# Kernel tuning notes

Measured on AMD Instinct MI355X. Metric: run time of the kernel, lower is better.

Reference implementation:

```python
import jax, jax.numpy as jnp
import numpy as np

L, H, D, DH, DFF, V, P, T, R = 12, 12, 768, 64, 3072, 30522, 512, 2, 50
RAT_LAYER = 6  # original condition: 5 < idx < 7


def layer_norm(x, g, b, eps=1e-12):
    m = x.mean(-1, keepdims=True)
    v = ((x - m) ** 2).mean(-1, keepdims=True)
    return (x - m) / jnp.sqrt(v + eps) * g + b


def setup_inputs() -> dict:
    key = jax.random.key(0)
    ks = iter(jax.random.split(key, 20))
    def n(shape, s=0.02):
        return jax.random.normal(next(ks), shape, dtype=jnp.float32) * s
    inp = dict(
        input_ids=jax.random.randint(next(ks), (4, 512), 0, V, dtype=jnp.int32),
        relations=jax.random.randint(next(ks), (4, 512, 512), 0, R, dtype=jnp.int32),
        attention_mask=jnp.ones((4, 512), dtype=jnp.int32),
        word_emb=n((V, D)), pos_emb=n((P, D)), type_emb=n((T, D)),
        emb_ln_g=jnp.ones((D,)), emb_ln_b=jnp.zeros((D,)),
        Wq=n((L, D, D)), bq=jnp.zeros((L, D)), Wk=n((L, D, D)), bk=jnp.zeros((L, D)),
        Wv=n((L, D, D)), bv=jnp.zeros((L, D)), Wo=n((L, D, D)), bo=jnp.zeros((L, D)),
        ln1_g=jnp.ones((L, D)), ln1_b=jnp.zeros((L, D)),
        Wi=n((L, D, DFF)), bi=jnp.zeros((L, DFF)),
        Wf=n((L, DFF, D)), bf=jnp.zeros((L, D)),
        ln2_g=jnp.ones((L, D)), ln2_b=jnp.zeros((L, D)),
        key_rel=n((L, R, DH)), val_rel=n((L, R, DH)),
        pool_w=n((D, D)), pool_b=jnp.zeros((D,)),
    )
    return inp


def reference(input_ids, relations, attention_mask, word_emb, pos_emb, type_emb,
              emb_ln_g, emb_ln_b, Wq, bq, Wk, bk, Wv, bv, Wo, bo, ln1_g, ln1_b,
              Wi, bi, Wf, bf, ln2_g, ln2_b, key_rel, val_rel, pool_w, pool_b):
    B, S = input_ids.shape
    # BERT embeddings (token_type_ids = zeros as in module default)
    h = word_emb[input_ids] + pos_emb[jnp.arange(S)][None] + type_emb[0][None, None]
    h = layer_norm(h, emb_ln_g, emb_ln_b)
    ext_mask = (1.0 - attention_mask.astype(jnp.float32))[:, None, None, :] * -10000.0
    inv_sqrt_dh = np.float32(1.0 / np.sqrt(DH))
    for i in range(L):
        q = (h @ Wq[i] + bq[i]).reshape(B, S, H, DH).transpose(0, 2, 1, 3)
        k = (h @ Wk[i] + bk[i]).reshape(B, S, H, DH).transpose(0, 2, 1, 3)
        v = (h @ Wv[i] + bv[i]).reshape(B, S, H, DH).transpose(0, 2, 1, 3)
        scores = jnp.einsum('bhsd,bhtd->bhst', q, k)
        if i == RAT_LAYER:
            kr = key_rel[i][relations]            # [B,S,S,DH] gathered relation keys
            scores = scores + jnp.einsum('bhsd,bstd->bhst', q, kr)
        scores = scores * inv_sqrt_dh + ext_mask
        probs = jax.nn.softmax(scores, axis=-1)   # dropout = identity (eval)
        ctx = jnp.einsum('bhst,bhtd->bhsd', probs, v)
        if i == RAT_LAYER:
            vr = val_rel[i][relations]            # [B,S,S,DH] gathered relation values
            ctx = ctx + jnp.einsum('bhst,bstd->bhsd', probs, vr)
        ctx = ctx.transpose(0, 2, 1, 3).reshape(B, S, D)
        attn_out = layer_norm(ctx @ Wo[i] + bo[i] + h, ln1_g[i], ln1_b[i])
        ff = jax.nn.gelu(attn_out @ Wi[i] + bi[i], approximate=False)
        h = layer_norm(ff @ Wf[i] + bf[i] + attn_out, ln2_g[i], ln2_b[i])
    pooled = jnp.tanh(h[:, 0] @ pool_w + pool_b)
    return h, pooled
```

## Files before the change

### kernel.cpp

```cpp
#include <hip/hip_runtime.h>
#include <math.h>

typedef unsigned short u16;
typedef unsigned int   u32;
typedef __bf16  bf16x8 __attribute__((ext_vector_type(8)));
typedef float   f32x4  __attribute__((ext_vector_type(4)));
typedef u16     u16x8  __attribute__((ext_vector_type(8)));

__device__ __forceinline__ u16 f2bf(float f) {
  u32 u = __builtin_bit_cast(u32, f);
  u32 r = (u + 0x7fffu + ((u >> 16) & 1u)) >> 16;
  return (u16)r;
}
__device__ __forceinline__ float bf2f(u16 h) {
  u32 u = ((u32)h) << 16;
  return __builtin_bit_cast(float, u);
}
__device__ __forceinline__ void gload16(const void* g, void* l) {
  __builtin_amdgcn_global_load_lds((const __attribute__((address_space(1))) void*)g,
                                   (__attribute__((address_space(3))) void*)l, 16, 0, 0);
}
__device__ __forceinline__ bf16x8 ld_bf8(const u16* p) {
  u16x8 v = *(const u16x8*)p;
  return __builtin_bit_cast(bf16x8, v);
}
__device__ __forceinline__ f32x4 mfma16(bf16x8 a, bf16x8 b, f32x4 c) {
  return __builtin_amdgcn_mfma_f32_16x16x32_bf16(a, b, c, 0, 0, 0);
}

struct ConvP {
  const float *wq, *wk, *wv, *wo, *wi, *wf;
  u16 *oqkv, *oo, *oi, *of;
};
__global__ __launch_bounds__(256) void conv_weights(ConvP p) {
  int t = blockIdx.x;
  const float* in; u16* out; int K, N, tn, tk;
  if (t < 1728) { int wh = t / 576, tt = t % 576;
    in = wh==0 ? p.wq : (wh==1 ? p.wk : p.wv);
    out = p.oqkv + (size_t)wh * 768 * 768;
    K = 768; N = 768; tn = tt % 24; tk = tt / 24;
  } else if (t < 2304) { int tt = t - 1728; in = p.wo; out = p.oo; K=768;  N=768;  tn=tt%24; tk=tt/24; }
  else if (t < 4608)   { int tt = t - 2304; in = p.wi; out = p.oi; K=768;  N=3072; tn=tt%96; tk=tt/96; }
  else                 { int tt = t - 4608; in = p.wf; out = p.of; K=3072; N=768;  tn=tt%24; tk=tt/24; }
  int n0 = tn*32, k0 = tk*32;
  __shared__ float tile[32][33];
  int x = threadIdx.x, y = threadIdx.y;
  #pragma unroll
  for (int j = 0; j < 4; ++j)
    tile[y + j*8][x] = in[(size_t)(k0 + y + j*8) * N + n0 + x];
  __syncthreads();
  #pragma unroll
  for (int j = 0; j < 4; ++j)
    out[(size_t)(n0 + y + j*8) * K + k0 + x] = f2bf(tile[x][y + j*8]);
}

struct GP {
  const u16* A; const u16* B;
  int K, N;
  long sA, sB, sOut;
  const float* bias; const float* res;
  float* outF; u16* outB;
  const float* bq; const float* bk; const float* bv;
  u16* qO; u16* kO; u16* vO;
};

template<int BM, int BN, int WAVES, int EPI, int KS>
__global__ __launch_bounds__(WAVES*64) void gemm_bt(GP p) {
  constexpr int THREADS = WAVES * 64;
  constexpr int WC = WAVES / 2;
  constexpr int WM = BM / 2, WN = BN / WC, MR = WM / 16, NR = WN / 16;
  constexpr int AIT = BM * 64 / (THREADS * 8);
  constexpr int BIT = BN * 64 / (THREADS * 8);
  const int tid = threadIdx.x;
  const int wave = tid >> 6, lane = tid & 63;
  const int wr = wave / WC, wc = wave % WC;
  const int wm0 = wr * WM, wn0 = wc * WN;
  const int bn = blockIdx.x, bm = blockIdx.y, bz = blockIdx.z;
  const int K = p.K;
  const int kLen = K / KS;
  const int kBeg = (KS > 1) ? bz * kLen : 0;
  const u16* A  = p.A + ((KS > 1) ? 0 : (size_t)bz * p.sA);
  const u16* Bp = p.B + ((KS > 1) ? 0 : (size_t)bz * p.sB);
  const int rowA0 = bm * BM, colB0 = bn * BN;

  __shared__ __align__(16) u16 lds[(BM + BN) * 64];
  u16* Al = lds; u16* Bl = lds + BM * 64;

  f32x4 acc[MR][NR];
  #pragma unroll
  for (int i = 0; i < MR; ++i)
    #pragma unroll
    for (int j = 0; j < NR; ++j) acc[i][j] = f32x4{0.f,0.f,0.f,0.f};

  for (int kt = kBeg; kt < kBeg + kLen; kt += 64) {
    #pragma unroll
    for (int it = 0; it < AIT; ++it) {
      int e = tid * 8 + it * THREADS * 8;
      gload16(A + (size_t)(rowA0 + (e >> 6)) * K + kt + (e & 63), Al + e);
    }
    #pragma unroll
    for (int it = 0; it < BIT; ++it) {
      int e = tid * 8 + it * THREADS * 8;
      gload16(Bp + (size_t)(colB0 + (e >> 6)) * K + kt + (e & 63), Bl + e);
    }
    __syncthreads();
    #pragma unroll
    for (int ks = 0; ks < 2; ++ks) {
      bf16x8 av[MR]; bf16x8 bw[NR];
      #pragma unroll
      for (int mf = 0; mf < MR; ++mf)
        av[mf] = ld_bf8(Al + (wm0 + mf*16 + (lane&15))*64 + ks*32 + (lane>>4)*8);
      #pragma unroll
      for (int nf = 0; nf < NR; ++nf)
        bw[nf] = ld_bf8(Bl + (wn0 + nf*16 + (lane&15))*64 + ks*32 + (lane>>4)*8);
      #pragma unroll
      for (int mf = 0; mf < MR; ++mf)
        #pragma unroll
        for (int nf = 0; nf < NR; ++nf)
          acc[mf][nf] = mfma16(av[mf], bw[nf], acc[mf][nf]);
    }
    __syncthreads();
  }

  #pragma unroll
  for (int mf = 0; mf < MR; ++mf) {
    #pragma unroll
    for (int nf = 0; nf < NR; ++nf) {
      int col = colB0 + wn0 + nf*16 + (lane & 15);
      #pragma unroll
      for (int reg = 0; reg < 4; ++reg) {
        int row = rowA0 + wm0 + mf*16 + (lane >> 4)*4 + reg;
        float v = acc[mf][nf][reg];
        if constexpr (EPI == 0) {
          int wh = col / 768, cc = col % 768;
          int hh = cc >> 6, d = col & 63;
          int b = row >> 9, s = row & 511;
          const float* bias = wh==0 ? p.bq : (wh==1 ? p.bk : p.bv);
          u16 o = f2bf(v + bias[cc]);
          if (wh == 0)      p.qO[((((size_t)b*12 + hh)*512 + s) << 6) + d] = o;
          else if (wh == 1) p.kO[((((size_t)b*12 + hh)*512 + s) << 6) + d] = o;
          else              p.vO[((((size_t)b*12 + hh)*64  + d) << 9) + s] = o;
        } else if constexpr (EPI == 1) {
          int b = bz / 12, hh = bz % 12;
          p.outB[((size_t)(b*512 + row))*768 + hh*64 + col] = f2bf(v);
        } else if constexpr (EPI == 2) {
          p.outF[(size_t)bz * p.sOut + (size_t)row * p.N + col] = v;
        } else if constexpr (EPI == 3) {
          float xg = v + p.bias[col];
          float gg = 0.5f * xg * (1.f + erff(xg * 0.70710678118f));
          p.outB[(size_t)row * p.N + col] = f2bf(gg);
        } else {
          p.outB[(size_t)bz * p.sOut + (size_t)row * p.N + col] = f2bf(v);
        }
      }
    }
  }
}

template<int RAT>
__global__ __launch_bounds__(256) void softmax_k(
    const u16* __restrict__ sc,
    const int* __restrict__ mask,
    u16* __restrict__ probs,
    const float* __restrict__ qr,
    const int* __restrict__ rel,
    float* __restrict__ wbins) {
  const int wave = threadIdx.x >> 6, lane = threadIdx.x & 63;
  const int row = blockIdx.x * 4 + wave;
  const int head = row >> 9, s = row & 511;
  const int b = head / 12;

  __shared__ float qlds[4][52];
  __shared__ float wlds[4][52];
  if constexpr (RAT) {
    if (lane < 52) {
      qlds[wave][lane] = (lane < 50) ? qr[(size_t)row*50 + lane] : 0.f;
      wlds[wave][lane] = 0.f;
    }
  }
  __syncthreads();

  u16x8 sv = *(const u16x8*)(sc + (size_t)row*512 + lane*8);
  const int* relrow = rel + ((size_t)(b*512 + s))*512 + lane*8;
  const int* mrow   = mask + b*512 + lane*8;

  float x[8];
  int rr[8];
  #pragma unroll
  for (int j = 0; j < 8; ++j) {
    float v = bf2f(sv[j]);
    if constexpr (RAT) { rr[j] = relrow[j]; v += qlds[wave][rr[j]]; }
    x[j] = v * 0.125f + -10000.f * (1.f - (float)mrow[j]);
  }

  float m = x[0];
  #pragma unroll
  for (int j = 1; j < 8; ++j) m = fmaxf(m, x[j]);
  #pragma unroll
  for (int o = 1; o < 64; o <<= 1) m = fmaxf(m, __shfl_xor(m, o));

  float sum = 0.f;
  #pragma unroll
  for (int j = 0; j < 8; ++j) { x[j] = __expf(x[j] - m); sum += x[j]; }
  #pragma unroll
  for (int o = 1; o < 64; o <<= 1) sum += __shfl_xor(sum, o);
  float inv = 1.f / sum;

  u16x8 ov;
  #pragma unroll
  for (int j = 0; j < 8; ++j) {
    float pv = x[j] * inv;
    ov[j] = f2bf(pv);
    if constexpr (RAT) atomicAdd(&wlds[wave][rr[j]], pv);
  }
  *(u16x8*)(probs + (size_t)row*512 + lane*8) = ov;

  if constexpr (RAT) {
    __syncthreads();
    if (lane < 50) wbins[(size_t)row*50 + lane] = wlds[wave][lane];
  }
}

__global__ __launch_bounds__(256) void rat_qr(const u16* __restrict__ q,
    const float* __restrict__ kr, float* __restrict__ qr) {
  int idx = blockIdx.x * 256 + threadIdx.x;
  if (idx >= 24576 * 50) return;
  int r = idx % 50; size_t bhs = (size_t)idx / 50;
  const u16* qp = q + bhs * 64;
  const float* kp = kr + r * 64;
  float acc = 0.f;
  #pragma unroll
  for (int d = 0; d < 64; ++d) acc += bf2f(qp[d]) * kp[d];
  qr[idx] = acc;
}

__global__ __launch_bounds__(256) void rat_apply(const float* __restrict__ wbins,
    const float* __restrict__ vr, u16* __restrict__ ctx) {
  __shared__ float vrl[50*64];
  __shared__ float wl[32*50];
  int tid = threadIdx.x;
  int rows0 = blockIdx.x * 32;
  for (int i = tid; i < 50*64; i += 256) vrl[i] = vr[i];
  for (int i = tid; i < 32*50; i += 256) wl[i] = wbins[(size_t)rows0*50 + i];
  __syncthreads();
  int wave = tid >> 6, lane = tid & 63;
  #pragma unroll
  for (int i = 0; i < 8; ++i) {
    int r = wave*8 + i;
    size_t idx = (size_t)rows0 + r;
    float acc = 0.f;
    #pragma unroll
    for (int j = 0; j < 50; ++j) acc += wl[r*50 + j] * vrl[j*64 + lane];
    int s = (int)(idx & 511); size_t bh = idx >> 9;
    int b = (int)(bh / 12), hh = (int)(bh % 12);
    u16* cp = ctx + ((size_t)(b*512 + s))*768 + hh*64 + lane;
    *cp = f2bf(bf2f(*cp) + acc);
  }
}

__global__ __launch_bounds__(256) void embed_ln(const int* __restrict__ ids,
    const float* __restrict__ we, const float* __restrict__ pe, const float* __restrict__ te,
    const float* __restrict__ g, const float* __restrict__ b,
    float* __restrict__ hF, u16* __restrict__ hB) {
  int row = blockIdx.x, tid = threadIdx.x;
  int s = row & 511;
  int id = ids[row];
  float x[3];
  #pragma unroll
  for (int j = 0; j < 3; ++j) {
    int d = tid + j*256;
    x[j] = we[(size_t)id*768 + d] + pe[(size_t)s*768 + d] + te[d];
  }
  __shared__ float red[4];
  float sm = x[0] + x[1] + x[2];
  #pragma unroll
  for (int o = 32; o; o >>= 1) sm += __shfl_xor(sm, o);
  if (!(tid & 63)) red[tid >> 6] = sm;
  __syncthreads();
  float mean = (red[0]+red[1]+red[2]+red[3]) * (1.f/768.f);
  __syncthreads();
  float q = 0.f;
  #pragma unroll
  for (int j = 0; j < 3; ++j) { float d = x[j] - mean; q += d*d; }
  #pragma unroll
  for (int o = 32; o; o >>= 1) q += __shfl_xor(q, o);
  if (!(tid & 63)) red[tid >> 6] = q;
  __syncthreads();
  float inv = rsqrtf((red[0]+red[1]+red[2]+red[3]) * (1.f/768.f) + 1e-12f);
  #pragma unroll
  for (int j = 0; j < 3; ++j) {
    int d = tid + j*256;
    float y = (x[j] - mean) * inv * g[d] + b[d];
    hF[(size_t)row*768 + d] = y;
    hB[(size_t)row*768 + d] = f2bf(y);
  }
}

__global__ __launch_bounds__(256) void ln_fused(const float* __restrict__ p0,
    const float* __restrict__ p1, const float* __restrict__ p2, const float* __restrict__ p3,
    int np, const float* __restrict__ bias, const float* __restrict__ res,
    const float* __restrict__ g, const float* __restrict__ b,
    float* __restrict__ oF, u16* __restrict__ oB) {
  int row = blockIdx.x, tid = threadIdx.x;
  size_t base = (size_t)row * 768;
  float v[3];
  #pragma unroll
  for (int j = 0; j < 3; ++j) {
    int d = tid + j*256;
    float x = p0[base + d];
    if (np > 1) x += p1[base + d];
    if (np > 2) x += p2[base + d];
    if (np > 3) x += p3[base + d];
    v[j] = x + bias[d] + res[base + d];
  }
  __shared__ float red[4];
  float sm = v[0] + v[1] + v[2];
  #pragma unroll
  for (int o = 32; o; o >>= 1) sm += __shfl_xor(sm, o);
  if (!(tid & 63)) red[tid >> 6] = sm;
  __syncthreads();
  float mean = (red[0]+red[1]+red[2]+red[3]) * (1.f/768.f);
  __syncthreads();
  float q = 0.f;
  #pragma unroll
  for (int j = 0; j < 3; ++j) { float d = v[j] - mean; q += d*d; }
  #pragma unroll
  for (int o = 32; o; o >>= 1) q += __shfl_xor(q, o);
  if (!(tid & 63)) red[tid >> 6] = q;
  __syncthreads();
  float inv = rsqrtf((red[0]+red[1]+red[2]+red[3]) * (1.f/768.f) + 1e-12f);
  #pragma unroll
  for (int j = 0; j < 3; ++j) {
    int d = tid + j*256;
    float y = (v[j] - mean) * inv * g[d] + b[d];
    oF[base + d] = y;
    oB[base + d] = f2bf(y);
  }
}

__global__ __launch_bounds__(256) void pooler_k(const float* __restrict__ h,
    const float* __restrict__ w, const float* __restrict__ bias, float* __restrict__ out) {
  int b = blockIdx.x, tid = threadIdx.x;
  __shared__ float hr[768];
  for (int i = tid; i < 768; i += 256) hr[i] = h[((size_t)b*512)*768 + i];
  __syncthreads();
  float a0 = 0.f, a1 = 0.f, a2 = 0.f;
  for (int kk = 0; kk < 768; ++kk) {
    float hv = hr[kk];
    const float* wr = w + (size_t)kk*768;
    a0 += hv * wr[tid]; a1 += hv * wr[tid+256]; a2 += hv * wr[tid+512];
  }
  out[(size_t)b*768 + tid]       = tanhf(a0 + bias[tid]);
  out[(size_t)b*768 + tid + 256] = tanhf(a1 + bias[tid+256]);
  out[(size_t)b*768 + tid + 512] = tanhf(a2 + bias[tid+512]);
}

__global__ __launch_bounds__(256) void copy_out(const float* __restrict__ in, float* __restrict__ out) {
  size_t i = ((size_t)blockIdx.x * 256 + threadIdx.x) * 4;
  *(float4*)(out + i) = *(const float4*)(in + i);
}

extern "C" void kernel_launch(void* const* d_in, const int* in_sizes, int n_in,
                              void* d_out, int out_size, void* d_ws, size_t ws_size,
                              hipStream_t stream) {
  const int*   ids   = (const int*)d_in[0];
  const int*   rel   = (const int*)d_in[1];
  const int*   amask = (const int*)d_in[2];
  const float* we    = (const float*)d_in[3];
  const float* pe    = (const float*)d_in[4];
  const float* te    = (const float*)d_in[5];
  const float* eg    = (const float*)d_in[6];
  const float* ebb   = (const float*)d_in[7];
  const float* Wq    = (const float*)d_in[8];
  const float* bq    = (const float*)d_in[9];
  const float* Wk    = (const float*)d_in[10];
  const float* bk    = (const float*)d_in[11];
  const float* Wv    = (const float*)d_in[12];
  const float* bv    = (const float*)d_in[13];
  const float* Wo    = (const float*)d_in[14];
  const float* bo    = (const float*)d_in[15];
  const float* g1    = (const float*)d_in[16];
  const float* b1    = (const float*)d_in[17];
  const float* Wi    = (const float*)d_in[18];
  const float* bi    = (const float*)d_in[19];
  const float* Wf    = (const float*)d_in[20];
  const float* bfp   = (const float*)d_in[21];
  const float* g2    = (const float*)d_in[22];
  const float* b2    = (const float*)d_in[23];
  const float* krel  = (const float*)d_in[24];
  const float* vrel  = (const float*)d_in[25];
  const float* pwp   = (const float*)d_in[26];
  const float* pbp   = (const float*)d_in[27];
  (void)in_sizes; (void)n_in; (void)out_size; (void)ws_size;

  char* ws = (char*)d_ws;
  size_t off = 0;
  auto take = [&](size_t bytes) { char* p = ws + off; off += (bytes + 255) & ~(size_t)255; return p; };
  u16*   wqkv = (u16*)take((size_t)2304*768*2);
  u16*   wo_l = (u16*)take((size_t)768*768*2);
  u16*   wi_l = (u16*)take((size_t)3072*768*2);
  u16*   wf_l = (u16*)take((size_t)768*3072*2);
  float* hF   = (float*)take((size_t)2048*768*4);
  u16*   hB   = (u16*)take((size_t)2048*768*2);
  float* atF  = (float*)take((size_t)2048*768*4);
  u16*   atB  = (u16*)take((size_t)2048*768*2);
  u16*   qB   = (u16*)take((size_t)2048*768*2);
  u16*   kB   = (u16*)take((size_t)2048*768*2);
  u16*   vB   = (u16*)take((size_t)2048*768*2);
  u16*   ctxB = (u16*)take((size_t)2048*768*2);
  char*  uni  = take((size_t)4*2048*768*4 + (size_t)2048*3072*2);
  float* tmpF = (float*)uni;
  u16*   scF  = (u16*)uni;
  u16*   ffB  = (u16*)(uni + (size_t)4*2048*768*4);
  u16*   prB  = (u16*)take((size_t)48*512*512*2);
  float* qrF  = (float*)take((size_t)24576*50*4);
  float* wbF  = (float*)take((size_t)24576*50*4);
  const size_t PSTRIDE = (size_t)2048*768;

  embed_ln<<<2048, 256, 0, stream>>>(ids, we, pe, te, eg, ebb, hF, hB);

  for (int l = 0; l < 12; ++l) {
    ConvP cp{Wq + (size_t)l*768*768, Wk + (size_t)l*768*768, Wv + (size_t)l*768*768,
             Wo + (size_t)l*768*768, Wi + (size_t)l*768*3072, Wf + (size_t)l*3072*768,
             wqkv, wo_l, wi_l, wf_l};
    conv_weights<<<6912, dim3(32,8), 0, stream>>>(cp);

    GP pq{}; pq.A = hB; pq.B = wqkv; pq.K = 768; pq.N = 2304;
    pq.bq = bq + l*768; pq.bk = bk + l*768; pq.bv = bv + l*768;
    pq.qO = qB; pq.kO = kB; pq.vO = vB;
    gemm_bt<128,128,8,0,1><<<dim3(18,16,1), 512, 0, stream>>>(pq);

    GP ps{}; ps.A = qB; ps.B = kB; ps.K = 64; ps.N = 512;
    ps.sA = 512*64; ps.sB = 512*64; ps.sOut = (long)512*512; ps.outB = scF;
    gemm_bt<128,128,8,4,1><<<dim3(4,4,48), 512, 0, stream>>>(ps);

    if (l == 6) {
      rat_qr<<<4800, 256, 0, stream>>>(qB, krel + 6*50*64, qrF);
      softmax_k<1><<<6144, 256, 0, stream>>>(scF, amask, prB, qrF, rel, wbF);
    } else {
      softmax_k<0><<<6144, 256, 0, stream>>>(scF, amask, prB, qrF, rel, wbF);
    }

    GP pc{}; pc.A = prB; pc.B = vB; pc.K = 512; pc.N = 64;
    pc.sA = (long)512*512; pc.sB = 64*512; pc.outB = ctxB;
    gemm_bt<64,64,4,1,1><<<dim3(1,8,48), 256, 0, stream>>>(pc);
    if (l == 6) rat_apply<<<768, 256, 0, stream>>>(wbF, vrel + 6*50*64, ctxB);

    GP po{}; po.A = ctxB; po.B = wo_l; po.K = 768; po.N = 768; po.sOut = PSTRIDE;
    po.outF = tmpF;
    gemm_bt<64,128,4,2,2><<<dim3(6,32,2), 256, 0, stream>>>(po);
    ln_fused<<<2048, 256, 0, stream>>>(tmpF, tmpF + PSTRIDE, nullptr, nullptr, 2,
                                       bo + l*768, hF, g1 + l*768, b1 + l*768, atF, atB);

    GP pf1{}; pf1.A = atB; pf1.B = wi_l; pf1.K = 768; pf1.N = 3072;
    pf1.bias = bi + (size_t)l*3072; pf1.outB = ffB;
    gemm_bt<128,128,8,3,1><<<dim3(24,16,1), 512, 0, stream>>>(pf1);

    GP pf2{}; pf2.A = ffB; pf2.B = wf_l; pf2.K = 3072; pf2.N = 768; pf2.sOut = PSTRIDE;
    pf2.outF = tmpF;
    gemm_bt<64,128,4,2,4><<<dim3(6,32,4), 256, 0, stream>>>(pf2);
    ln_fused<<<2048, 256, 0, stream>>>(tmpF, tmpF + PSTRIDE, tmpF + 2*PSTRIDE, tmpF + 3*PSTRIDE, 4,
                                       bfp + l*768, atF, g2 + l*768, b2 + l*768, hF, hB);
  }

  copy_out<<<1536, 256, 0, stream>>>(hF, (float*)d_out);
  pooler_k<<<4, 256, 0, stream>>>(hF, pwp, pbp, (float*)d_out + (size_t)2048*768);
}
```

Measured before the change: 2.003 ms.

## Fuse QK^T, softmax and PV into a flash-attention kernel for non-RAT layers

For the 11 layers without relation-aware attention, a single flash-style kernel replaces the separate score GEMM, softmax and PV GEMM. It computes scores with MFMA, keeps an online softmax in registers, stages probabilities through LDS and accumulates the context directly. This avoids writing and reading the 48x512x512 score and probability buffers in HBM and cuts kernel launches. In exchange there are only 384 blocks with no load/compute pipelining, and the ffB buffer is split out of the union because scF is now written only in layer 6.

Result: faster. 1.914 ms (-4.4%).

```diff
diff --git a/kernel.cpp b/kernel.cpp
--- a/kernel.cpp
+++ b/kernel.cpp
@@ -157,14 +157,140 @@
   }
 }
 
+__global__ __launch_bounds__(256) void flash_attn(
+    const u16* __restrict__ q, const u16* __restrict__ k, const u16* __restrict__ v,
+    const int* __restrict__ mask, u16* __restrict__ ctx) {
+  const int head = blockIdx.x;
+  const int bm = blockIdx.y;
+  const int b = head / 12, hh = head % 12;
+  const int tid = threadIdx.x, wave = tid >> 6, lane = tid & 63;
+  const int row0 = bm * 64;
+  const u16* qb = q + (size_t)head * 512 * 64;
+  const u16* kb = k + (size_t)head * 512 * 64;
+  const u16* vb = v + (size_t)head * 64 * 512;
+
+  __shared__ __align__(16) u16 Ql[64*64];
+  __shared__ __align__(16) u16 Kl[64*64];
+  __shared__ __align__(16) u16 Vl[64*64];
+  __shared__ __align__(16) u16 pw[4][16*72];
+  __shared__ float em_lds[512];
+
+  for (int i = tid; i < 512; i += 256)
+    em_lds[i] = -10000.f * (1.f - (float)mask[b*512 + i]);
+
+  #pragma unroll
+  for (int it = 0; it < 2; ++it) {
+    int e = tid*8 + it*2048;
+    gload16(qb + (size_t)(row0 + (e>>6))*64 + (e&63), Ql + e);
+  }
+  __syncthreads();
+  bf16x8 qf[2];
+  #pragma unroll
+  for (int ks = 0; ks < 2; ++ks)
+    qf[ks] = ld_bf8(Ql + (wave*16 + (lane&15))*64 + ks*32 + (lane>>4)*8);
+
+  f32x4 ctxacc[4];
+  #pragma unroll
+  for (int nf = 0; nf < 4; ++nf) ctxacc[nf] = f32x4{0.f,0.f,0.f,0.f};
+  float mrun[4], lrun[4];
+  #pragma unroll
+  for (int r = 0; r < 4; ++r) { mrun[r] = -3.0e38f; lrun[r] = 0.f; }
+
+  for (int t0 = 0; t0 < 512; t0 += 64) {
+    __syncthreads();
+    #pragma unroll
+    for (int it = 0; it < 2; ++it) {
+      int e = tid*8 + it*2048;
+      gload16(kb + (size_t)(t0 + (e>>6))*64 + (e&63), Kl + e);
+    }
+    #pragma unroll
+    for (int it = 0; it < 2; ++it) {
+      int e = tid*8 + it*2048;
+      gload16(vb + (size_t)(e>>6)*512 + t0 + (e&63), Vl + e);
+    }
+    __syncthreads();
+
+    f32x4 s[4];
+    #pragma unroll
+    for (int nf = 0; nf < 4; ++nf) s[nf] = f32x4{0.f,0.f,0.f,0.f};
+    #pragma unroll
+    for (int ks = 0; ks < 2; ++ks)
+      #pragma unroll
+      for (int nf = 0; nf < 4; ++nf) {
+        bf16x8 kf = ld_bf8(Kl + (nf*16 + (lane&15))*64 + ks*32 + (lane>>4)*8);
+        s[nf] = mfma16(qf[ks], kf, s[nf]);
+      }
+
+    float em4[4];
+    #pragma unroll
+    for (int nf = 0; nf < 4; ++nf) em4[nf] = em_lds[t0 + nf*16 + (lane&15)];
+
+    float scale_[4];
+    #pragma unroll
+    for (int reg = 0; reg < 4; ++reg) {
+      float pm = -3.0e38f;
+      #pragma unroll
+      for (int nf = 0; nf < 4; ++nf) {
+        s[nf][reg] = s[nf][reg]*0.125f + em4[nf];
+        pm = fmaxf(pm, s[nf][reg]);
+      }
+      #pragma unroll
+      for (int o = 1; o < 16; o <<= 1) pm = fmaxf(pm, __shfl_xor(pm, o));
+      float mnew = fmaxf(mrun[reg], pm);
+      float sc = __expf(mrun[reg] - mnew);
+      mrun[reg] = mnew;
+      scale_[reg] = sc;
+      float lsum = 0.f;
+      #pragma unroll
+      for (int nf = 0; nf < 4; ++nf) {
+        float e = __expf(s[nf][reg] - mnew);
+        s[nf][reg] = e;
+        lsum += e;
+      }
+      #pragma unroll
+      for (int o = 1; o < 16; o <<= 1) lsum += __shfl_xor(lsum, o);
+      lrun[reg] = lrun[reg]*sc + lsum;
+    }
+
+    #pragma unroll
+    for (int nf = 0; nf < 4; ++nf)
+      #pragma unroll
+      for (int reg = 0; reg < 4; ++reg) {
+        int qq = (lane>>4)*4 + reg;
+        pw[wave][qq*72 + nf*16 + (lane&15)] = f2bf(s[nf][reg]);
+      }
+
+    #pragma unroll
+    for (int nf = 0; nf < 4; ++nf)
+      #pragma unroll
+      for (int reg = 0; reg < 4; ++reg)
+        ctxacc[nf][reg] *= scale_[reg];
+    #pragma unroll
+    for (int ks = 0; ks < 2; ++ks) {
+      bf16x8 pf = ld_bf8(pw[wave] + (lane&15)*72 + ks*32 + (lane>>4)*8);
+      #pragma unroll
+      for (int nf = 0; nf < 4; ++nf) {
+        bf16x8 vf = ld_bf8(Vl + (nf*16 + (lane&15))*64 + ks*32 + (lane>>4)*8);
+        ctxacc[nf] = mfma16(pf, vf, ctxacc[nf]);
+      }
+    }
+  }
+
+  #pragma unroll
+  for (int nf = 0; nf < 4; ++nf)
+    #pragma unroll
+    for (int reg = 0; reg < 4; ++reg) {
+      int qg = row0 + wave*16 + (lane>>4)*4 + reg;
+      int d  = nf*16 + (lane&15);
+      ctx[((size_t)(b*512 + qg))*768 + hh*64 + d] = f2bf(ctxacc[nf][reg] / lrun[reg]);
+    }
+}
+
 template<int RAT>
 __global__ __launch_bounds__(256) void softmax_k(
-    const u16* __restrict__ sc,
-    const int* __restrict__ mask,
-    u16* __restrict__ probs,
-    const float* __restrict__ qr,
-    const int* __restrict__ rel,
-    float* __restrict__ wbins) {
+    const u16* __restrict__ sc, const int* __restrict__ mask,
+    u16* __restrict__ probs, const float* __restrict__ qr,
+    const int* __restrict__ rel, float* __restrict__ wbins) {
   const int wave = threadIdx.x >> 6, lane = threadIdx.x & 63;
   const int row = blockIdx.x * 4 + wave;
   const int head = row >> 9, s = row & 511;
@@ -408,10 +534,10 @@
   u16*   kB   = (u16*)take((size_t)2048*768*2);
   u16*   vB   = (u16*)take((size_t)2048*768*2);
   u16*   ctxB = (u16*)take((size_t)2048*768*2);
-  char*  uni  = take((size_t)4*2048*768*4 + (size_t)2048*3072*2);
+  char*  uni  = take((size_t)4*2048*768*4);
   float* tmpF = (float*)uni;
   u16*   scF  = (u16*)uni;
-  u16*   ffB  = (u16*)(uni + (size_t)4*2048*768*4);
+  u16*   ffB  = (u16*)take((size_t)2048*3072*2);
   u16*   prB  = (u16*)take((size_t)48*512*512*2);
   float* qrF  = (float*)take((size_t)24576*50*4);
   float* wbF  = (float*)take((size_t)24576*50*4);
@@ -430,21 +556,19 @@
     pq.qO = qB; pq.kO = kB; pq.vO = vB;
     gemm_bt<128,128,8,0,1><<<dim3(18,16,1), 512, 0, stream>>>(pq);
 
-    GP ps{}; ps.A = qB; ps.B = kB; ps.K = 64; ps.N = 512;
-    ps.sA = 512*64; ps.sB = 512*64; ps.sOut = (long)512*512; ps.outB = scF;
-    gemm_bt<128,128,8,4,1><<<dim3(4,4,48), 512, 0, stream>>>(ps);
-
     if (l == 6) {
+      GP ps{}; ps.A = qB; ps.B = kB; ps.K = 64; ps.N = 512;
+      ps.sA = 512*64; ps.sB = 512*64; ps.sOut = (long)512*512; ps.outB = scF;
+      gemm_bt<128,128,8,4,1><<<dim3(4,4,48), 512, 0, stream>>>(ps);
       rat_qr<<<4800, 256, 0, stream>>>(qB, krel + 6*50*64, qrF);
       softmax_k<1><<<6144, 256, 0, stream>>>(scF, amask, prB, qrF, rel, wbF);
+      GP pc{}; pc.A = prB; pc.B = vB; pc.K = 512; pc.N = 64;
+      pc.sA = (long)512*512; pc.sB = 64*512; pc.outB = ctxB;
+      gemm_bt<64,64,4,1,1><<<dim3(1,8,48), 256, 0, stream>>>(pc);
+      rat_apply<<<768, 256, 0, stream>>>(wbF, vrel + 6*50*64, ctxB);
     } else {
-      softmax_k<0><<<6144, 256, 0, stream>>>(scF, amask, prB, qrF, rel, wbF);
-    }
-
-    GP pc{}; pc.A = prB; pc.B = vB; pc.K = 512; pc.N = 64;
-    pc.sA = (long)512*512; pc.sB = 64*512; pc.outB = ctxB;
-    gemm_bt<64,64,4,1,1><<<dim3(1,8,48), 256, 0, stream>>>(pc);
-    if (l == 6) rat_apply<<<768, 256, 0, stream>>>(wbF, vrel + 6*50*64, ctxB);
+      flash_attn<<<dim3(48,8), 256, 0, stream>>>(qB, kB, vB, amask, ctxB);
+    }
 
     GP po{}; po.A = ctxB; po.B = wo_l; po.K = 768; po.N = 768; po.sOut = PSTRIDE;
     po.outF = tmpF;
```
